# Kernel tuning notes

Measured on AMD Instinct MI355X. Metric: run time of the kernel, lower is better.

Reference implementation:

```python
import jax, jax.numpy as jnp
import numpy as np

EPS = 1e-5


def _segment_norm(x, seg, num_segments):
    # x: [N, D], seg: [N] sorted segment ids in [0, num_segments)
    ones = jnp.ones((x.shape[0],), x.dtype)
    cnt = jax.ops.segment_sum(ones, seg, num_segments=num_segments)      # [B]
    safe = jnp.maximum(cnt, 1.0)[:, None]                                # avoid 0-div
    mean = jax.ops.segment_sum(x, seg, num_segments=num_segments) / safe # [B, D]
    centered = x - mean[seg]
    var = jax.ops.segment_sum(centered * centered, seg, num_segments=num_segments) / safe
    std = jnp.sqrt(var)                                                  # unbiased=False
    normed = centered / (std[seg] + EPS)
    # graphs with a single element are passed through unchanged
    return jnp.where((cnt > 1.0)[seg][:, None], normed, x)


def setup_inputs() -> dict:
    key = jax.random.key(0)
    k1, k2, k3, k4 = jax.random.split(key, 4)
    N, D, B = 1_000_000, 128, 1024
    node_feat = jax.random.normal(k1, (N, D), dtype=jnp.float32)
    edge_feat = jax.random.normal(k2, (N, D), dtype=jnp.float32)
    node_seg = jnp.sort(jax.random.randint(k3, (N,), 0, B, dtype=jnp.int32))
    edge_seg = jnp.sort(jax.random.randint(k4, (N,), 0, B, dtype=jnp.int32))
    return {
        "node_feat": node_feat,
        "edge_feat": edge_feat,
        "node_gamma": jnp.ones((D,), jnp.float32),
        "node_beta": jnp.zeros((D,), jnp.float32),
        "edge_gamma": jnp.ones((D,), jnp.float32),
        "edge_beta": jnp.zeros((D,), jnp.float32),
        "node_seg": node_seg,
        "edge_seg": edge_seg,
        "num_graphs": B,
    }


def reference(node_feat, edge_feat, node_gamma, node_beta, edge_gamma, edge_beta,
              node_seg, edge_seg, num_graphs):
    node_out = _segment_norm(node_feat, node_seg, num_graphs) * node_gamma + node_beta
    edge_out = _segment_norm(edge_feat, edge_seg, num_graphs) * edge_gamma + edge_beta
    return (node_out, edge_out)
```

## Files before the change

### kernel.cpp

```cpp
#include <hip/hip_runtime.h>


static constexpr int   D4  = 32;
static constexpr float EPS = 1e-5f;

__global__ __launch_bounds__(256) void seg_norm_kernel(
    const float4* __restrict__ xn, const float4* __restrict__ xe,
    const float*  __restrict__ gn, const float*  __restrict__ bn,
    const float*  __restrict__ ge, const float*  __restrict__ be,
    const int*    __restrict__ sn, const int*    __restrict__ se,
    float4* __restrict__ on, float4* __restrict__ oe,
    int N)
{
    const bool is_edge = (blockIdx.y != 0);
    const float4* __restrict__ x   = is_edge ? xe : xn;
    const float*  __restrict__ gam = is_edge ? ge : gn;
    const float*  __restrict__ bet = is_edge ? be : bn;
    const int*    __restrict__ seg = is_edge ? se : sn;
    float4*       __restrict__ out = is_edge ? oe : on;

    const int b   = (int)blockIdx.x;
    const int tid = (int)threadIdx.x;

    __shared__ int s_bounds[2];
    if (tid < 2) {
        const int target = b + tid;
        int lo = 0, hi = N;
        while (lo < hi) {
            int mid = (lo + hi) >> 1;
            if (seg[mid] < target) lo = mid + 1; else hi = mid;
        }
        s_bounds[tid] = lo;
    }
    __syncthreads();
    const int start = s_bounds[0];
    const int end   = s_bounds[1];
    const int cnt   = end - start;
    if (cnt <= 0) return;

    const int lane = tid & 31;
    const int rg   = tid >> 5;

    float4 s = {0.f, 0.f, 0.f, 0.f};
    float4 q = {0.f, 0.f, 0.f, 0.f};
    for (int r = start + rg; r < end; r += 8) {
        const float4 v = x[(size_t)r * D4 + lane];
        s.x += v.x; s.y += v.y; s.z += v.z; s.w += v.w;
        q.x += v.x * v.x; q.y += v.y * v.y;
        q.z += v.z * v.z; q.w += v.w * v.w;
    }

    __shared__ float4 redS[256];
    __shared__ float4 redQ[256];
    redS[tid] = s;
    redQ[tid] = q;
    __syncthreads();

    if (tid < 32) {
        float4 S = redS[tid];
        float4 Q = redQ[tid];
        #pragma unroll
        for (int k = 1; k < 8; ++k) {
            const float4 a = redS[k * 32 + tid];
            const float4 c = redQ[k * 32 + tid];
            S.x += a.x; S.y += a.y; S.z += a.z; S.w += a.w;
            Q.x += c.x; Q.y += c.y; Q.z += c.z; Q.w += c.w;
        }
        const float rc = 1.0f / (float)cnt;
        float4 m, iv;
        m.x = S.x * rc; m.y = S.y * rc; m.z = S.z * rc; m.w = S.w * rc;
        float vx = fmaxf(Q.x * rc - m.x * m.x, 0.f);
        float vy = fmaxf(Q.y * rc - m.y * m.y, 0.f);
        float vz = fmaxf(Q.z * rc - m.z * m.z, 0.f);
        float vw = fmaxf(Q.w * rc - m.w * m.w, 0.f);
        iv.x = 1.0f / (sqrtf(vx) + EPS);
        iv.y = 1.0f / (sqrtf(vy) + EPS);
        iv.z = 1.0f / (sqrtf(vz) + EPS);
        iv.w = 1.0f / (sqrtf(vw) + EPS);
        if (cnt <= 1) {
            m.x = m.y = m.z = m.w = 0.f;
            iv.x = iv.y = iv.z = iv.w = 1.f;
        }
        const float4 g4 = ((const float4*)gam)[tid];
        const float4 b4 = ((const float4*)bet)[tid];
        float4 A, Bc;
        A.x = iv.x * g4.x; A.y = iv.y * g4.y;
        A.z = iv.z * g4.z; A.w = iv.w * g4.w;
        Bc.x = b4.x - m.x * A.x; Bc.y = b4.y - m.y * A.y;
        Bc.z = b4.z - m.z * A.z; Bc.w = b4.w - m.w * A.w;
        redS[tid] = A;
        redQ[tid] = Bc;
    }
    __syncthreads();

    const float4 A  = redS[lane];
    const float4 Bc = redQ[lane];

    for (int r = start + rg; r < end; r += 8) {
        const size_t idx = (size_t)r * D4 + lane;
        const float4 v = x[idx];
        float4 o;
        o.x = v.x * A.x + Bc.x;
        o.y = v.y * A.y + Bc.y;
        o.z = v.z * A.z + Bc.z;
        o.w = v.w * A.w + Bc.w;
        out[idx] = o;
    }
}

extern "C" void kernel_launch(void* const* d_in, const int* in_sizes, int n_in,
                              void* d_out, int out_size, void* d_ws, size_t ws_size,
                              hipStream_t stream) {
    const float* node_feat  = (const float*)d_in[0];
    const float* edge_feat  = (const float*)d_in[1];
    const float* node_gamma = (const float*)d_in[2];
    const float* node_beta  = (const float*)d_in[3];
    const float* edge_gamma = (const float*)d_in[4];
    const float* edge_beta  = (const float*)d_in[5];
    const int*   node_seg   = (const int*)d_in[6];
    const int*   edge_seg   = (const int*)d_in[7];

    const int D = in_sizes[2];
    const int N = in_sizes[0] / D;
    const int B = 1024;

    float* out_node = (float*)d_out;
    float* out_edge = out_node + (size_t)N * (size_t)D;

    dim3 grid((unsigned)B, 2);
    seg_norm_kernel<<<grid, 256, 0, stream>>>(
        (const float4*)node_feat, (const float4*)edge_feat,
        node_gamma, node_beta, edge_gamma, edge_beta,
        node_seg, edge_seg,
        (float4*)out_node, (float4*)out_edge, N);
}
```

Before: 609.7 us.

## Pipeline segment stats pass with normalize pass across four segments per block

Each block now handles two node segments and two edge segments. While it normalizes and writes one segment, it reads the next segment's rows to accumulate that segment's statistics, so the stats read and the apply pass overlap in one loop. Output writes use nontemporal stores. The grid shrinks to 512 blocks. That halves parallelism and adds serial dependence within each block, so latency hiding may suffer.

```diff
diff --git a/kernel.cpp b/kernel.cpp
--- a/kernel.cpp
+++ b/kernel.cpp
@@ -4,7 +4,20 @@
 static constexpr int   D4  = 32;
 static constexpr float EPS = 1e-5f;
 
-__global__ __launch_bounds__(256) void seg_norm_kernel(
+typedef float vfloat4 __attribute__((ext_vector_type(4)));
+
+__device__ __forceinline__ void nt_store4(float4* p, const float4& v) {
+    vfloat4 w = { v.x, v.y, v.z, v.w };
+    __builtin_nontemporal_store(w, reinterpret_cast<vfloat4*>(p));
+}
+
+__device__ __forceinline__ void acc4(float4& s, float4& q, const float4& v) {
+    s.x += v.x; s.y += v.y; s.z += v.z; s.w += v.w;
+    q.x += v.x * v.x; q.y += v.y * v.y;
+    q.z += v.z * v.z; q.w += v.w * v.w;
+}
+
+__global__ __launch_bounds__(256) void seg_norm_pipe(
     const float4* __restrict__ xn, const float4* __restrict__ xe,
     const float*  __restrict__ gn, const float*  __restrict__ bn,
     const float*  __restrict__ ge, const float*  __restrict__ be,
@@ -12,99 +25,118 @@
     float4* __restrict__ on, float4* __restrict__ oe,
     int N)
 {
-    const bool is_edge = (blockIdx.y != 0);
-    const float4* __restrict__ x   = is_edge ? xe : xn;
-    const float*  __restrict__ gam = is_edge ? ge : gn;
-    const float*  __restrict__ bet = is_edge ? be : bn;
-    const int*    __restrict__ seg = is_edge ? se : sn;
-    float4*       __restrict__ out = is_edge ? oe : on;
+    const int k    = (int)blockIdx.x;
+    const int tid  = (int)threadIdx.x;
+    const int lane = tid & 31;
+    const int rg   = tid >> 5;
 
-    const int b   = (int)blockIdx.x;
-    const int tid = (int)threadIdx.x;
+    __shared__ int    sb[8];
+    __shared__ float4 redS[256], redQ[256];
+    __shared__ float4 sA[32], sBc[32];
 
-    __shared__ int s_bounds[2];
-    if (tid < 2) {
-        const int target = b + tid;
+    if (tid < 8) {
+        const int t      = tid >> 1;
+        const int* sg    = (t < 2) ? sn : se;
+        const int target = 2 * k + (t & 1) + (tid & 1);
         int lo = 0, hi = N;
         while (lo < hi) {
             int mid = (lo + hi) >> 1;
-            if (seg[mid] < target) lo = mid + 1; else hi = mid;
+            if (sg[mid] < target) lo = mid + 1; else hi = mid;
         }
-        s_bounds[tid] = lo;
-    }
-    __syncthreads();
-    const int start = s_bounds[0];
-    const int end   = s_bounds[1];
-    const int cnt   = end - start;
-    if (cnt <= 0) return;
-
-    const int lane = tid & 31;
-    const int rg   = tid >> 5;
-
-    float4 s = {0.f, 0.f, 0.f, 0.f};
-    float4 q = {0.f, 0.f, 0.f, 0.f};
-    for (int r = start + rg; r < end; r += 8) {
-        const float4 v = x[(size_t)r * D4 + lane];
-        s.x += v.x; s.y += v.y; s.z += v.z; s.w += v.w;
-        q.x += v.x * v.x; q.y += v.y * v.y;
-        q.z += v.z * v.z; q.w += v.w * v.w;
-    }
-
-    __shared__ float4 redS[256];
-    __shared__ float4 redQ[256];
-    redS[tid] = s;
-    redQ[tid] = q;
-    __syncthreads();
-
-    if (tid < 32) {
-        float4 S = redS[tid];
-        float4 Q = redQ[tid];
-        #pragma unroll
-        for (int k = 1; k < 8; ++k) {
-            const float4 a = redS[k * 32 + tid];
-            const float4 c = redQ[k * 32 + tid];
-            S.x += a.x; S.y += a.y; S.z += a.z; S.w += a.w;
-            Q.x += c.x; Q.y += c.y; Q.z += c.z; Q.w += c.w;
-        }
-        const float rc = 1.0f / (float)cnt;
-        float4 m, iv;
-        m.x = S.x * rc; m.y = S.y * rc; m.z = S.z * rc; m.w = S.w * rc;
-        float vx = fmaxf(Q.x * rc - m.x * m.x, 0.f);
-        float vy = fmaxf(Q.y * rc - m.y * m.y, 0.f);
-        float vz = fmaxf(Q.z * rc - m.z * m.z, 0.f);
-        float vw = fmaxf(Q.w * rc - m.w * m.w, 0.f);
-        iv.x = 1.0f / (sqrtf(vx) + EPS);
-        iv.y = 1.0f / (sqrtf(vy) + EPS);
-        iv.z = 1.0f / (sqrtf(vz) + EPS);
-        iv.w = 1.0f / (sqrtf(vw) + EPS);
-        if (cnt <= 1) {
-            m.x = m.y = m.z = m.w = 0.f;
-            iv.x = iv.y = iv.z = iv.w = 1.f;
-        }
-        const float4 g4 = ((const float4*)gam)[tid];
-        const float4 b4 = ((const float4*)bet)[tid];
-        float4 A, Bc;
-        A.x = iv.x * g4.x; A.y = iv.y * g4.y;
-        A.z = iv.z * g4.z; A.w = iv.w * g4.w;
-        Bc.x = b4.x - m.x * A.x; Bc.y = b4.y - m.y * A.y;
-        Bc.z = b4.z - m.z * A.z; Bc.w = b4.w - m.w * A.w;
-        redS[tid] = A;
-        redQ[tid] = Bc;
+        sb[tid] = lo;
     }
     __syncthreads();
 
-    const float4 A  = redS[lane];
-    const float4 Bc = redQ[lane];
+    float4 s = make_float4(0.f, 0.f, 0.f, 0.f);
+    float4 q = make_float4(0.f, 0.f, 0.f, 0.f);
 
-    for (int r = start + rg; r < end; r += 8) {
-        const size_t idx = (size_t)r * D4 + lane;
-        const float4 v = x[idx];
-        float4 o;
-        o.x = v.x * A.x + Bc.x;
-        o.y = v.y * A.y + Bc.y;
-        o.z = v.z * A.z + Bc.z;
-        o.w = v.w * A.w + Bc.w;
-        out[idx] = o;
+    {
+        const int st = sb[0], en = sb[1];
+        for (int r = st + rg; r < en; r += 8)
+            acc4(s, q, xn[(size_t)r * D4 + lane]);
+    }
+
+    #pragma unroll 4
+    for (int t = 0; t < 4; ++t) {
+        const float4* __restrict__ xp = (t < 2) ? xn : xe;
+        float4*       __restrict__ op = (t < 2) ? on : oe;
+        const float*  __restrict__ gm = (t < 2) ? gn : ge;
+        const float*  __restrict__ bt = (t < 2) ? bn : be;
+        const int stp = sb[2 * t], enp = sb[2 * t + 1];
+        const int cnt = enp - stp;
+
+        __syncthreads();
+        redS[tid] = s; redQ[tid] = q;
+        __syncthreads();
+        if (tid < 32) {
+            float4 S = redS[tid], Q = redQ[tid];
+            #pragma unroll
+            for (int j = 1; j < 8; ++j) {
+                const float4 a = redS[j * 32 + tid];
+                const float4 c = redQ[j * 32 + tid];
+                S.x += a.x; S.y += a.y; S.z += a.z; S.w += a.w;
+                Q.x += c.x; Q.y += c.y; Q.z += c.z; Q.w += c.w;
+            }
+            const float rcnt = 1.0f / (float)max(cnt, 1);
+            float4 m, iv;
+            m.x = S.x * rcnt; m.y = S.y * rcnt; m.z = S.z * rcnt; m.w = S.w * rcnt;
+            const float vx = fmaxf(Q.x * rcnt - m.x * m.x, 0.f);
+            const float vy = fmaxf(Q.y * rcnt - m.y * m.y, 0.f);
+            const float vz = fmaxf(Q.z * rcnt - m.z * m.z, 0.f);
+            const float vw = fmaxf(Q.w * rcnt - m.w * m.w, 0.f);
+            iv.x = 1.0f / (sqrtf(vx) + EPS);
+            iv.y = 1.0f / (sqrtf(vy) + EPS);
+            iv.z = 1.0f / (sqrtf(vz) + EPS);
+            iv.w = 1.0f / (sqrtf(vw) + EPS);
+            if (cnt <= 1) {
+                m.x = m.y = m.z = m.w = 0.f;
+                iv.x = iv.y = iv.z = iv.w = 1.f;
+            }
+            const float4 g4 = ((const float4*)gm)[tid];
+            const float4 b4 = ((const float4*)bt)[tid];
+            float4 A, Bc;
+            A.x = iv.x * g4.x; A.y = iv.y * g4.y;
+            A.z = iv.z * g4.z; A.w = iv.w * g4.w;
+            Bc.x = b4.x - m.x * A.x; Bc.y = b4.y - m.y * A.y;
+            Bc.z = b4.z - m.z * A.z; Bc.w = b4.w - m.w * A.w;
+            sA[tid] = A; sBc[tid] = Bc;
+        }
+        __syncthreads();
+        const float4 A  = sA[lane];
+        const float4 Bc = sBc[lane];
+
+        int stc = 0, enc = 0;
+        const float4* __restrict__ xc = xn;
+        if (t < 3) {
+            xc  = (t == 0) ? xn : xe;
+            stc = sb[2 * t + 2];
+            enc = sb[2 * t + 3];
+        }
+
+        s = make_float4(0.f, 0.f, 0.f, 0.f);
+        q = make_float4(0.f, 0.f, 0.f, 0.f);
+
+        int rp  = stp + rg;
+        int rcl = stc + rg;
+        float4 vc = make_float4(0.f, 0.f, 0.f, 0.f);
+        bool pend = false;
+        if (rcl < enc) { vc = xc[(size_t)rcl * D4 + lane]; pend = true; rcl += 8; }
+        while (rp < enp || pend) {
+            float4 vp; const bool hp = (rp < enp);
+            if (hp) vp = xp[(size_t)rp * D4 + lane];
+            float4 vc2 = make_float4(0.f, 0.f, 0.f, 0.f);
+            bool pend2 = false;
+            if (rcl < enc) { vc2 = xc[(size_t)rcl * D4 + lane]; pend2 = true; rcl += 8; }
+            if (hp) {
+                float4 o;
+                o.x = vp.x * A.x + Bc.x; o.y = vp.y * A.y + Bc.y;
+                o.z = vp.z * A.z + Bc.z; o.w = vp.w * A.w + Bc.w;
+                nt_store4(&op[(size_t)rp * D4 + lane], o);
+                rp += 8;
+            }
+            if (pend) acc4(s, q, vc);
+            vc = vc2; pend = pend2;
+        }
     }
 }
 
@@ -127,8 +159,8 @@
     float* out_node = (float*)d_out;
     float* out_edge = out_node + (size_t)N * (size_t)D;
 
-    dim3 grid((unsigned)B, 2);
-    seg_norm_kernel<<<grid, 256, 0, stream>>>(
+    dim3 grid((unsigned)(B / 2));
+    seg_norm_pipe<<<grid, 256, 0, stream>>>(
         (const float4*)node_feat, (const float4*)edge_feat,
         node_gamma, node_beta, edge_gamma, edge_beta,
         node_seg, edge_seg,
```

Result: slower. 644.5 us (+5.7%).

## Double-buffer segment reads via async global-to-LDS loads with nontemporal stores

Applied to the files above, without the earlier changes.

Both passes over each segment now stream the rows through per-wave double-buffered LDS staging using global_load_lds, with explicit vmcnt waits so the next tile's load overlaps the current tile's compute. The output is written with nontemporal stores to avoid polluting the cache. Each segment is treated as a flat float4 stream with a scalar tail loop. The aim is more memory-level parallelism on a bandwidth-bound kernel. The cost is hand-written waitcnt accounting, which is fragile: the vmcnt values must also count the outstanding stores in the second pass.

```diff
diff --git a/kernel.cpp b/kernel.cpp
--- a/kernel.cpp
+++ b/kernel.cpp
@@ -1,10 +1,30 @@
 #include <hip/hip_runtime.h>
 
 
-static constexpr int   D4  = 32;
-static constexpr float EPS = 1e-5f;
+static constexpr int   D4     = 32;
+static constexpr int   CHUNK  = 64;
+static constexpr int   NCHUNK = 4;
+static constexpr int   TILE_W = CHUNK * NCHUNK;
+static constexpr int   TILE_B = TILE_W * 4;
+static constexpr float EPS    = 1e-5f;
 
-__global__ __launch_bounds__(256) void seg_norm_kernel(
+typedef float vfloat4 __attribute__((ext_vector_type(4)));
+
+#define WAITV(N) do { asm volatile("s_waitcnt vmcnt(" #N ")" ::: "memory"); \
+                      __builtin_amdgcn_sched_barrier(0); } while (0)
+
+__device__ __forceinline__ void nt_store4(float4* p, const float4& v) {
+    vfloat4 w = { v.x, v.y, v.z, v.w };
+    __builtin_nontemporal_store(w, reinterpret_cast<vfloat4*>(p));
+}
+
+__device__ __forceinline__ void acc4(float4& s, float4& q, const float4& v) {
+    s.x += v.x; s.y += v.y; s.z += v.z; s.w += v.w;
+    q.x += v.x * v.x; q.y += v.y * v.y;
+    q.z += v.z * v.z; q.w += v.w * v.w;
+}
+
+__global__ __launch_bounds__(256) void seg_norm_async(
     const float4* __restrict__ xn, const float4* __restrict__ xe,
     const float*  __restrict__ gn, const float*  __restrict__ bn,
     const float*  __restrict__ ge, const float*  __restrict__ be,
@@ -12,6 +32,10 @@
     float4* __restrict__ on, float4* __restrict__ oe,
     int N)
 {
+    __shared__ float4 stage[4][2][TILE_W];
+    __shared__ float4 redS[256], redQ[256];
+    __shared__ int    s_bounds[2];
+
     const bool is_edge = (blockIdx.y != 0);
     const float4* __restrict__ x   = is_edge ? xe : xn;
     const float*  __restrict__ gam = is_edge ? ge : gn;
@@ -22,7 +46,6 @@
     const int b   = (int)blockIdx.x;
     const int tid = (int)threadIdx.x;
 
-    __shared__ int s_bounds[2];
     if (tid < 2) {
         const int target = b + tid;
         int lo = 0, hi = N;
@@ -38,27 +61,46 @@
     const int cnt   = end - start;
     if (cnt <= 0) return;
 
-    const int lane = tid & 31;
-    const int rg   = tid >> 5;
+    const int w    = tid >> 6;
+    const int lane = tid & 63;
+    const int dg   = tid & 31;
 
-    float4 s = {0.f, 0.f, 0.f, 0.f};
-    float4 q = {0.f, 0.f, 0.f, 0.f};
-    for (int r = start + rg; r < end; r += 8) {
-        const float4 v = x[(size_t)r * D4 + lane];
-        s.x += v.x; s.y += v.y; s.z += v.z; s.w += v.w;
-        q.x += v.x * v.x; q.y += v.y * v.y;
-        q.z += v.z * v.z; q.w += v.w * v.w;
+    const size_t f4base = (size_t)start * D4;
+    const int    f4cnt  = cnt * D4;
+    const int    nt     = f4cnt / TILE_B;
+
+    float4* const sb0 = &stage[w][0][0];
+    float4* const sb1 = &stage[w][1][0];
+
+    auto issue = [&](int t, float4* lp) {
+        const float4* gp = x + f4base + (size_t)t * TILE_B + w * TILE_W + lane;
+        #pragma unroll
+        for (int i = 0; i < NCHUNK; ++i)
+            __builtin_amdgcn_global_load_lds(gp + i * CHUNK, lp + i * CHUNK, 16, 0, 0);
+    };
+
+    float4 s = make_float4(0.f, 0.f, 0.f, 0.f);
+    float4 q = make_float4(0.f, 0.f, 0.f, 0.f);
+    if (nt > 0) {
+        issue(0, sb0);
+        for (int t = 0; t < nt; ++t) {
+            float4* cur = (t & 1) ? sb1 : sb0;
+            float4* nxt = (t & 1) ? sb0 : sb1;
+            if (t + 1 < nt) { issue(t + 1, nxt); WAITV(4); }
+            else            { WAITV(0); }
+            #pragma unroll
+            for (int i = 0; i < NCHUNK; ++i)
+                acc4(s, q, cur[i * CHUNK + lane]);
+        }
     }
+    for (int j = nt * TILE_B + tid; j < f4cnt; j += 256)
+        acc4(s, q, x[f4base + j]);
 
-    __shared__ float4 redS[256];
-    __shared__ float4 redQ[256];
-    redS[tid] = s;
-    redQ[tid] = q;
+    redS[tid] = s; redQ[tid] = q;
     __syncthreads();
 
     if (tid < 32) {
-        float4 S = redS[tid];
-        float4 Q = redQ[tid];
+        float4 S = redS[tid], Q = redQ[tid];
         #pragma unroll
         for (int k = 1; k < 8; ++k) {
             const float4 a = redS[k * 32 + tid];
@@ -69,10 +111,10 @@
         const float rc = 1.0f / (float)cnt;
         float4 m, iv;
         m.x = S.x * rc; m.y = S.y * rc; m.z = S.z * rc; m.w = S.w * rc;
-        float vx = fmaxf(Q.x * rc - m.x * m.x, 0.f);
-        float vy = fmaxf(Q.y * rc - m.y * m.y, 0.f);
-        float vz = fmaxf(Q.z * rc - m.z * m.z, 0.f);
-        float vw = fmaxf(Q.w * rc - m.w * m.w, 0.f);
+        const float vx = fmaxf(Q.x * rc - m.x * m.x, 0.f);
+        const float vy = fmaxf(Q.y * rc - m.y * m.y, 0.f);
+        const float vz = fmaxf(Q.z * rc - m.z * m.z, 0.f);
+        const float vw = fmaxf(Q.w * rc - m.w * m.w, 0.f);
         iv.x = 1.0f / (sqrtf(vx) + EPS);
         iv.y = 1.0f / (sqrtf(vy) + EPS);
         iv.z = 1.0f / (sqrtf(vz) + EPS);
@@ -88,23 +130,39 @@
         A.z = iv.z * g4.z; A.w = iv.w * g4.w;
         Bc.x = b4.x - m.x * A.x; Bc.y = b4.y - m.y * A.y;
         Bc.z = b4.z - m.z * A.z; Bc.w = b4.w - m.w * A.w;
-        redS[tid] = A;
-        redQ[tid] = Bc;
+        redS[tid] = A; redQ[tid] = Bc;
     }
     __syncthreads();
+    const float4 A  = redS[dg];
+    const float4 Bc = redQ[dg];
+    __syncthreads();
 
-    const float4 A  = redS[lane];
-    const float4 Bc = redQ[lane];
-
-    for (int r = start + rg; r < end; r += 8) {
-        const size_t idx = (size_t)r * D4 + lane;
-        const float4 v = x[idx];
+    if (nt > 0) {
+        issue(0, sb0);
+        for (int t = 0; t < nt; ++t) {
+            float4* cur = (t & 1) ? sb1 : sb0;
+            float4* nxt = (t & 1) ? sb0 : sb1;
+            const bool hn = (t + 1 < nt);
+            if (hn) issue(t + 1, nxt);
+            if (t == 0) { if (hn) WAITV(4); else WAITV(0); }
+            else        { if (hn) WAITV(8); else WAITV(4); }
+            float4* op = out + f4base + (size_t)t * TILE_B + w * TILE_W + lane;
+            #pragma unroll
+            for (int i = 0; i < NCHUNK; ++i) {
+                const float4 v = cur[i * CHUNK + lane];
+                float4 o;
+                o.x = v.x * A.x + Bc.x; o.y = v.y * A.y + Bc.y;
+                o.z = v.z * A.z + Bc.z; o.w = v.w * A.w + Bc.w;
+                nt_store4(op + i * CHUNK, o);
+            }
+        }
+    }
+    for (int j = nt * TILE_B + tid; j < f4cnt; j += 256) {
+        const float4 v = x[f4base + j];
         float4 o;
-        o.x = v.x * A.x + Bc.x;
-        o.y = v.y * A.y + Bc.y;
-        o.z = v.z * A.z + Bc.z;
-        o.w = v.w * A.w + Bc.w;
-        out[idx] = o;
+        o.x = v.x * A.x + Bc.x; o.y = v.y * A.y + Bc.y;
+        o.z = v.z * A.z + Bc.z; o.w = v.w * A.w + Bc.w;
+        nt_store4(&((float4*)out)[f4base + j], o);
     }
 }
 
@@ -128,7 +186,7 @@
     float* out_edge = out_node + (size_t)N * (size_t)D;
 
     dim3 grid((unsigned)B, 2);
-    seg_norm_kernel<<<grid, 256, 0, stream>>>(
+    seg_norm_async<<<grid, 256, 0, stream>>>(
         (const float4*)node_feat, (const float4*)edge_feat,
         node_gamma, node_beta, edge_gamma, edge_beta,
         node_seg, edge_seg,
```

Measured after the change: 569.1 us. -6.7%, faster.
